# Kernel tuning notes

Hardware: AMD Instinct MI355X
Metric: run time of the kernel (lower is better)

## Reference

```python
import jax, jax.numpy as jnp
import numpy as np

N, E, F, H, L, G, EMB, C = 50000, 600000, 128, 128, 4, 64, 64, 10
BN_EPS = 1e-5


def setup_inputs() -> dict:
    key = jax.random.key(0)
    k = lambda i: jax.random.fold_in(key, i)
    s = 0.05  # weight scale
    return {
        "x": jax.random.normal(k(0), (N, F), jnp.float32),
        "edge_index": jax.random.randint(k(1), (2, E), 0, N, jnp.int64),
        "batch": jnp.sort(jax.random.randint(k(2), (N,), 0, G, jnp.int64)),
        "emb": jax.random.normal(k(3), (G, EMB), jnp.float32),
        "eps": jnp.zeros((L,), jnp.float32),
        "W1": jax.random.normal(k(4), (L, F, H), jnp.float32) * s,
        "b1": jnp.zeros((L, H), jnp.float32),
        "W2": jax.random.normal(k(5), (L, H, H), jnp.float32) * s,
        "b2": jnp.zeros((L, H), jnp.float32),
        "gamma": jnp.ones((L, H), jnp.float32),
        "beta": jnp.zeros((L, H), jnp.float32),
        "lin1_w": jax.random.normal(k(6), (L * H + EMB, 2 * H), jnp.float32) * s,
        "lin1_b": jnp.zeros((2 * H,), jnp.float32),
        "lin2_w": jax.random.normal(k(7), (2 * H, H), jnp.float32) * s,
        "lin2_b": jnp.zeros((H,), jnp.float32),
        "lin4_w": jax.random.normal(k(8), (H, C), jnp.float32) * s,
        "lin4_b": jnp.zeros((C,), jnp.float32),
    }


def _gin_mlp(h, W1, b1, W2, b2, gamma, beta):
    # Linear -> ReLU -> Linear -> ReLU -> BatchNorm1d (batch stats)
    h = jax.nn.relu(h @ W1 + b1)
    h = jax.nn.relu(h @ W2 + b2)
    mean = jnp.mean(h, axis=0)
    var = jnp.var(h, axis=0)
    return (h - mean) * jax.lax.rsqrt(var + BN_EPS) * gamma + beta


def reference(x, edge_index, batch, emb, eps, W1, b1, W2, b2, gamma, beta,
              lin1_w, lin1_b, lin2_w, lin2_b, lin4_w, lin4_b):
    src, dst = edge_index[0], edge_index[1]
    xs = []
    for l in range(L):
        # GIN: MLP((1+eps)*x_i + sum_{j->i} x_j)  via gather + scatter-add
        agg = jax.ops.segment_sum(x[src], dst, num_segments=N)  # [N,H]
        x = _gin_mlp((1.0 + eps[l]) * x + agg,
                     W1[l], b1[l], W2[l], b2[l], gamma[l], beta[l])
        xs.append(x)
    h = jnp.concatenate(xs, axis=1)  # [N, L*H]
    # global mean pool per graph
    sums = jax.ops.segment_sum(h, batch, num_segments=G)  # [G, L*H]
    cnt = jax.ops.segment_sum(jnp.ones((N,), h.dtype), batch, num_segments=G)
    pooled = sums / jnp.maximum(cnt, 1.0)[:, None]
    z = jnp.concatenate([pooled, emb.reshape(G, -1)], axis=1)
    z = jax.nn.relu(z @ lin1_w + lin1_b)  # .relu() twice is idempotent
    # dropout p=0.5 skipped (eval mode); lin3 unused in original forward
    z = jax.nn.relu(z @ lin2_w + lin2_b)
    z = z @ lin4_w + lin4_b
    return jax.nn.log_softmax(z, axis=1)
```

## Files before the change

### kernel.cpp

```cpp
#include <hip/hip_runtime.h>
#include <cstdint>
#include <cstddef>

#define N_NODES 50000
#define N_EDGES 600000
#define NLAYER  4
#define NGRAPH  64
#define STRIDE  64
#define NBANK   64
#define NBLK_MLP ((N_NODES + 127) / 128)
#define CVTX_NB ((N_NODES * 32 + 255) / 256)
#define CVTW_NB ((NLAYER * 128 * 128 * 2) / 256)
#define EDG_NB  ((N_EDGES + 255) / 256)

typedef unsigned int   u32;
typedef unsigned short u16;
typedef unsigned char  u8;
typedef float f32x4  __attribute__((ext_vector_type(4)));
typedef short bf16x8 __attribute__((ext_vector_type(8)));

__device__ __forceinline__ u16 f2bf(float f) {
    u32 x = __float_as_uint(f);
    u32 r = x + 0x7fffu + ((x >> 16) & 1u);
    return (u16)(r >> 16);
}
__device__ __forceinline__ u32 pack2(float a, float b) {
    return (u32)f2bf(a) | ((u32)f2bf(b) << 16);
}

__device__ __forceinline__ float fp8b0(u32 u) { return __builtin_amdgcn_cvt_f32_fp8(u, 0); }
__device__ __forceinline__ float fp8b1(u32 u) { return __builtin_amdgcn_cvt_f32_fp8(u, 1); }
__device__ __forceinline__ u32 pk_fp8(float a, float b) {
    return (u32)__builtin_amdgcn_cvt_pk_fp8_f32(a, b, 0, false);
}

__global__ __launch_bounds__(256) void setup_all(
    const float4* __restrict__ x, u32* __restrict__ xf8,
    const float* __restrict__ W1, const float* __restrict__ W2,
    short* __restrict__ W1t, short* __restrict__ W2t,
    const int* __restrict__ src, const int* __restrict__ dst,
    int* __restrict__ cnt, u16* __restrict__ col) {
    int b = blockIdx.x, tid = threadIdx.x;
    if (b < EDG_NB) {
        int e = b * 256 + tid;
        if (e < N_EDGES) {
            int d = dst[e];
            int pos = atomicAdd(&cnt[d], 1);
            if (pos < STRIDE) col[d * STRIDE + pos] = (u16)src[e];
        }
    } else if (b < EDG_NB + CVTX_NB) {
        int i = (b - EDG_NB) * 256 + tid;
        if (i < N_NODES * 32) {
            float4 v = x[i];
            u32 r = pk_fp8(v.x, v.y);
            r = (u32)__builtin_amdgcn_cvt_pk_fp8_f32(v.z, v.w, (int)r, true);
            xf8[i] = r;
        }
    } else {
        int i = (b - EDG_NB - CVTX_NB) * 256 + tid;
        int z = i >> 16, r = i & 65535;
        int l = r >> 14, n = (r >> 7) & 127, k = r & 127;
        const float* W = z ? W2 : W1;
        short* Wt      = z ? W2t : W1t;
        Wt[((size_t)l * 128 + n) * 128 + k] = (short)f2bf(W[((size_t)l * 128 + k) * 128 + n]);
    }
}

__global__ __launch_bounds__(256) void agg_kernel(
    const u16* __restrict__ xin,
    const float* __restrict__ coef,
    const int* __restrict__ cnt, const u16* __restrict__ col,
    const float* __restrict__ eps_all, int layer,
    u32* __restrict__ agg) {
    int node = blockIdx.x * 4 + (threadIdx.x >> 6);
    int lane = threadIdx.x & 63;
    if (node >= N_NODES) return;
    float a0 = 1.f, a1 = 1.f, d0 = 0.f, d1 = 0.f;
    if (coef) {
        a0 = coef[2 * lane];       a1 = coef[2 * lane + 1];
        d0 = coef[128 + 2 * lane]; d1 = coef[128 + 2 * lane + 1];
    }
    float ep = 1.0f + eps_all[layer];
    u32 v = xin[(size_t)node * 64 + lane];
    int dgc = min(cnt[node], STRIDE);
    int k0 = node * STRIDE, k1 = k0 + dgc;
    float s0 = 0.f, s1 = 0.f;
    int k = k0;
    int cc[8];
    if (k < k1) {
#pragma unroll
        for (int t = 0; t < 8; t++) cc[t] = col[min(k + t, k1 - 1)];
    }
    while (k < k1) {
        int idx[8];
#pragma unroll
        for (int t = 0; t < 8; t++) idx[t] = cc[t];
        int kn = k + 8;
        if (kn < k1) {
#pragma unroll
            for (int t = 0; t < 8; t++) cc[t] = col[min(kn + t, k1 - 1)];
        }
#pragma unroll
        for (int t = 0; t < 8; t++) {
            u32 u = xin[(size_t)idx[t] * 64 + lane];
            float w = (k + t < k1) ? 1.f : 0.f;
            s0 += w * fp8b0(u); s1 += w * fp8b1(u);
        }
        k = kn;
    }
    float deg = (float)dgc;
    float r0 = ep * (a0 * fp8b0(v) + d0) + a0 * s0 + deg * d0;
    float r1 = ep * (a1 * fp8b1(v) + d1) + a1 * s1 + deg * d1;
    agg[(size_t)node * 64 + lane] = pack2(r0, r1);
}

#define H1_STRIDE 136
#define WSTR      132
__global__ __launch_bounds__(256) void mlp_fused(
    const short* __restrict__ A,
    const short* __restrict__ W1t, const float* __restrict__ b1,
    const short* __restrict__ W2t, const float* __restrict__ b2,
    u8* __restrict__ H2, const int* __restrict__ batch,
    float* __restrict__ sumsB, float* __restrict__ gsum, int M) {
    __shared__ alignas(16) short wbuf[128 * WSTR];
    __shared__ alignas(16) short h1s[128 * H1_STRIDE];
    __shared__ int sh_ga, sh_gb, sh_split;
    int tid  = threadIdx.x;
    int wave = tid >> 6, lane = tid & 63;
    int ln15 = lane & 15, quad = lane >> 4;
    int m0blk = blockIdx.x * 128;
    int m0 = m0blk + wave * 32;
    const bf16x8 zz = {0, 0, 0, 0, 0, 0, 0, 0};

    if (tid == 0) {
        int rlo = m0blk, rhi = min(m0blk + 127, M - 1);
        int ga = batch[rlo], gb = batch[rhi];
        int split = m0blk + 128;
        if (ga != gb) {
            int lo = rlo, hi = rhi;
            while (lo + 1 < hi) { int mid = (lo + hi) >> 1; if (batch[mid] == ga) lo = mid; else hi = mid; }
            split = hi;
        }
        sh_ga = ga; sh_gb = gb; sh_split = split;
    }

    bf16x8 a[2][4];
#pragma unroll
    for (int rt = 0; rt < 2; rt++) {
        int row = m0 + rt * 16 + ln15;
        const short* rp = A + (size_t)row * 128 + quad * 8;
        bool ok = row < M;
#pragma unroll
        for (int s = 0; s < 4; s++)
            a[rt][s] = ok ? *(const bf16x8*)(rp + s * 32) : zz;
    }
    bf16x8 wr1[8], wr2[8];
#pragma unroll
    for (int i = 0; i < 8; i++)
        wr1[i] = *(const bf16x8*)(W1t + (size_t)(i * 256 + tid) * 8);
#pragma unroll
    for (int i = 0; i < 8; i++)
        wr2[i] = *(const bf16x8*)(W2t + (size_t)(i * 256 + tid) * 8);

#pragma unroll
    for (int i = 0; i < 8; i++) {
        int idx = i * 256 + tid;
        *(bf16x8*)&wbuf[(idx >> 4) * WSTR + (idx & 15) * 8] = wr1[i];
    }
    __syncthreads();

#pragma unroll
    for (int ct = 0; ct < 8; ct++) {
        const short* wp = &wbuf[(ct * 16 + ln15) * WSTR + quad * 8];
        bf16x8 b[4];
#pragma unroll
        for (int s = 0; s < 4; s++) b[s] = *(const bf16x8*)(wp + s * 32);
        float bias = b1[ct * 16 + ln15];
#pragma unroll
        for (int rt = 0; rt < 2; rt++) {
            f32x4 acc = {0.f, 0.f, 0.f, 0.f};
#pragma unroll
            for (int s = 0; s < 4; s++)
                acc = __builtin_amdgcn_mfma_f32_16x16x32_bf16(a[rt][s], b[s], acc, 0, 0, 0);
#pragma unroll
            for (int i = 0; i < 4; i++) {
                float v = fmaxf(acc[i] + bias, 0.f);
                int lr = wave * 32 + rt * 16 + quad * 4 + i;
                h1s[lr * H1_STRIDE + ct * 16 + ln15] = (short)f2bf(v);
            }
        }
    }
    __syncthreads();

#pragma unroll
    for (int i = 0; i < 8; i++) {
        int idx = i * 256 + tid;
        *(bf16x8*)&wbuf[(idx >> 4) * WSTR + (idx & 15) * 8] = wr2[i];
    }
    bf16x8 c[2][4];
#pragma unroll
    for (int rt = 0; rt < 2; rt++) {
        const short* rp = h1s + (size_t)(wave * 32 + rt * 16 + ln15) * H1_STRIDE + quad * 8;
#pragma unroll
        for (int s = 0; s < 4; s++) c[rt][s] = *(const bf16x8*)(rp + s * 32);
    }
    __syncthreads();

    int gsplit = sh_split;
    float sAcc[8], qAcc[8], pAcc[8];
#pragma unroll
    for (int ct = 0; ct < 8; ct++) { sAcc[ct] = 0.f; qAcc[ct] = 0.f; pAcc[ct] = 0.f; }
#pragma unroll
    for (int ct = 0; ct < 8; ct++) {
        const short* wp = &wbuf[(ct * 16 + ln15) * WSTR + quad * 8];
        bf16x8 b[4];
#pragma unroll
        for (int s = 0; s < 4; s++) b[s] = *(const bf16x8*)(wp + s * 32);
        float bias = b2[ct * 16 + ln15];
#pragma unroll
        for (int rt = 0; rt < 2; rt++) {
            f32x4 acc = {0.f, 0.f, 0.f, 0.f};
#pragma unroll
            for (int s = 0; s < 4; s++)
                acc = __builtin_amdgcn_mfma_f32_16x16x32_bf16(c[rt][s], b[s], acc, 0, 0, 0);
            int colx = ct * 16 + ln15;
#pragma unroll
            for (int i = 0; i < 4; i++) {
                int row = m0 + rt * 16 + quad * 4 + i;
                float v = fmaxf(acc[i] + bias, 0.f);
                if (row < M) H2[(size_t)row * 128 + colx] = (u8)(pk_fp8(v, v) & 0xffu);
                float vm = (row < M) ? v : 0.f;
                sAcc[ct] += vm; qAcc[ct] += vm * vm;
                if (row < gsplit) pAcc[ct] += vm;
            }
        }
    }
    __syncthreads();
    float* scr = (float*)h1s;
    int slice = wave * 4 + quad;
#pragma unroll
    for (int ct = 0; ct < 8; ct++) {
        int colx = ct * 16 + ln15;
        scr[(0 * 16 + slice) * 128 + colx] = sAcc[ct];
        scr[(1 * 16 + slice) * 128 + colx] = qAcc[ct];
        scr[(2 * 16 + slice) * 128 + colx] = pAcc[ct];
    }
    __syncthreads();
    if (tid < 128) {
        float ss = 0.f, qq = 0.f, pa = 0.f;
#pragma unroll
        for (int sl = 0; sl < 16; sl++) {
            ss += scr[(0 * 16 + sl) * 128 + tid];
            qq += scr[(1 * 16 + sl) * 128 + tid];
            pa += scr[(2 * 16 + sl) * 128 + tid];
        }
        float* sb = sumsB + (size_t)(blockIdx.x & (NBANK - 1)) * 256;
        atomicAdd(&sb[tid], ss);
        atomicAdd(&sb[128 + tid], qq);
        int ga = sh_ga, gb = sh_gb;
        atomicAdd(&gsum[ga * 128 + tid], pa);
        if (gb != ga) atomicAdd(&gsum[gb * 128 + tid], ss - pa);
    }
}

__global__ __launch_bounds__(128) void coef_fin(
    const float* __restrict__ sumsB,
    const float* __restrict__ gamma, const float* __restrict__ beta,
    int layer, float* __restrict__ coef) {
    int t = threadIdx.x;
    float s1 = 0.f, s2 = 0.f;
    for (int b = 0; b < NBANK; b++) {
        s1 += sumsB[b * 256 + t];
        s2 += sumsB[b * 256 + 128 + t];
    }
    float mean = s1 * (1.0f / N_NODES);
    float var  = s2 * (1.0f / N_NODES) - mean * mean;
    float a = rsqrtf(var + 1e-5f) * gamma[layer * 128 + t];
    coef[t]       = a;
    coef[128 + t] = beta[layer * 128 + t] - mean * a;
}

__global__ __launch_bounds__(256) void head_kernel(
    const float* __restrict__ gsum, const float* __restrict__ coefL,
    const int* __restrict__ batch, const float* __restrict__ emb,
    const float* __restrict__ l1w, const float* __restrict__ l1b,
    const float* __restrict__ l2w, const float* __restrict__ l2b,
    const float* __restrict__ l4w, const float* __restrict__ l4b,
    float* __restrict__ out) {
    __shared__ float z[576];
    __shared__ float z1[256];
    __shared__ float z2h[2][128];
    __shared__ float z2[128];
    __shared__ float zr[128][10];
    __shared__ float inv_cnt;
    int g = blockIdx.x;
    int tid = threadIdx.x;
    if (tid == 0) {
        int lo = 0, hi = N_NODES;
        while (lo < hi) { int m = (lo + hi) >> 1; if (batch[m] < g) lo = m + 1; else hi = m; }
        int s = lo;
        lo = 0; hi = N_NODES;
        while (lo < hi) { int m = (lo + hi) >> 1; if (batch[m] < g + 1) lo = m + 1; else hi = m; }
        inv_cnt = 1.0f / fmaxf((float)(lo - s), 1.0f);
    }
    __syncthreads();
    for (int j = tid; j < 512; j += 256) {
        int l = j >> 7, c = j & 127;
        float a = coefL[l * 256 + c], d = coefL[l * 256 + 128 + c];
        z[j] = a * gsum[(size_t)l * NGRAPH * 128 + g * 128 + c] * inv_cnt + d;
    }
    if (tid < 64) z[512 + tid] = emb[g * 64 + tid];
    __syncthreads();
    {
        float acc = l1b[tid];
        for (int j0 = 0; j0 < 576; j0 += 16) {
            float lw[16];
#pragma unroll
            for (int t = 0; t < 16; t++) lw[t] = l1w[(j0 + t) * 256 + tid];
#pragma unroll
            for (int t = 0; t < 16; t++) acc += z[j0 + t] * lw[t];
        }
        z1[tid] = fmaxf(acc, 0.f);
    }
    __syncthreads();
    {
        int c2 = tid & 127, half = tid >> 7;
        float acc = 0.f;
        int jb = half * 128;
        for (int j0 = 0; j0 < 128; j0 += 8) {
            float lw[8];
#pragma unroll
            for (int t = 0; t < 8; t++) lw[t] = l2w[(jb + j0 + t) * 128 + c2];
#pragma unroll
            for (int t = 0; t < 8; t++) acc += z1[jb + j0 + t] * lw[t];
        }
        z2h[half][c2] = acc;
    }
    __syncthreads();
    if (tid < 128) z2[tid] = fmaxf(z2h[0][tid] + z2h[1][tid] + l2b[tid], 0.f);
    __syncthreads();
    if (tid < 128) {
        float zv = z2[tid];
        const float* wr = l4w + tid * 10;
#pragma unroll
        for (int c = 0; c < 10; c++) zr[tid][c] = zv * wr[c];
    }
    __syncthreads();
    for (int s = 64; s >= 1; s >>= 1) {
        if (tid < s) {
#pragma unroll
            for (int c = 0; c < 10; c++) zr[tid][c] += zr[tid + s][c];
        }
        __syncthreads();
    }
    if (tid == 0) {
        float z3s[10];
#pragma unroll
        for (int c = 0; c < 10; c++) z3s[c] = zr[0][c] + l4b[c];
        float m = z3s[0];
        for (int i = 1; i < 10; i++) m = fmaxf(m, z3s[i]);
        float se = 0.f;
        for (int i = 0; i < 10; i++) se += expf(z3s[i] - m);
        float lse = m + logf(se);
        for (int i = 0; i < 10; i++) out[g * 10 + i] = z3s[i] - lse;
    }
}

extern "C" void kernel_launch(void* const* d_in, const int* in_sizes, int n_in,
                              void* d_out, int out_size, void* d_ws, size_t ws_size,
                              hipStream_t stream) {
    (void)in_sizes; (void)n_in; (void)out_size; (void)ws_size;
    const float* x0   = (const float*)d_in[0];
    const int* ei     = (const int*)d_in[1];
    const int* src    = ei;
    const int* dst    = ei + N_EDGES;
    const int* batch  = (const int*)d_in[2];
    const float* emb  = (const float*)d_in[3];
    const float* eps  = (const float*)d_in[4];
    const float* W1   = (const float*)d_in[5];
    const float* b1   = (const float*)d_in[6];
    const float* W2   = (const float*)d_in[7];
    const float* b2   = (const float*)d_in[8];
    const float* gamma= (const float*)d_in[9];
    const float* beta = (const float*)d_in[10];
    const float* l1w  = (const float*)d_in[11];
    const float* l1b  = (const float*)d_in[12];
    const float* l2w  = (const float*)d_in[13];
    const float* l2b  = (const float*)d_in[14];
    const float* l4w  = (const float*)d_in[15];
    const float* l4b  = (const float*)d_in[16];

    char* ws = (char*)d_ws;
    size_t off = 0;
    auto alloc = [&](size_t bytes) -> char* {
        char* p = ws + off; off += (bytes + 255) & ~(size_t)255; return p;
    };
    int* cnt    = (int*)alloc(N_NODES * 4);
    float* sumsB = (float*)alloc((size_t)NLAYER * NBANK * 256 * 4);
    float* gsumL = (float*)alloc((size_t)NLAYER * NGRAPH * 128 * 4);
    size_t zero_len = (char*)gsumL - (char*)cnt + (size_t)NLAYER * NGRAPH * 128 * 4;
    u16* col    = (u16*)alloc((size_t)N_NODES * STRIDE * 2);
    u8* xf8     = (u8*)alloc((size_t)N_NODES * 128);
    u8* h2a     = (u8*)alloc((size_t)N_NODES * 128);
    u8* h2b     = (u8*)alloc((size_t)N_NODES * 128);
    u32* agg    = (u32*)alloc((size_t)N_NODES * 64 * 4);
    short* W1t  = (short*)alloc((size_t)NLAYER * 128 * 128 * 2);
    short* W2t  = (short*)alloc((size_t)NLAYER * 128 * 128 * 2);
    float* coefL = (float*)alloc(NLAYER * 256 * 4);

    hipMemsetAsync(cnt, 0, zero_len, stream);

    setup_all<<<EDG_NB + CVTX_NB + CVTW_NB, 256, 0, stream>>>(
        (const float4*)x0, (u32*)xf8, W1, W2, W1t, W2t, src, dst, cnt, col);

    const u8* xin = xf8;
    for (int l = 0; l < NLAYER; ++l) {
        u8* h2 = (l & 1) ? h2b : h2a;
        const float* coef_prev = (l == 0) ? nullptr : (coefL + (l - 1) * 256);
        agg_kernel<<<(N_NODES + 3) / 4, 256, 0, stream>>>(
            (const u16*)xin, coef_prev, cnt, col, eps, l, agg);
        mlp_fused<<<NBLK_MLP, 256, 0, stream>>>(
            (const short*)agg, W1t + (size_t)l * 16384, b1 + l * 128,
            W2t + (size_t)l * 16384, b2 + l * 128, h2, batch,
            sumsB + (size_t)l * NBANK * 256, gsumL + (size_t)l * NGRAPH * 128, N_NODES);
        coef_fin<<<1, 128, 0, stream>>>(sumsB + (size_t)l * NBANK * 256,
                                        gamma, beta, l, coefL + l * 256);
        xin = h2;
    }
    head_kernel<<<NGRAPH, 256, 0, stream>>>(gsumL, coefL, batch, emb,
                                            l1w, l1b, l2w, l2b, l4w, l4b,
                                            (float*)d_out);
}
```

Measured before the change: 378.5 us.

## Split wave into four neighbor groups with 8-byte gathers and shuffle reduction

The aggregation kernel now has each wave work on four neighbor rows at once. Each 16-lane group gathers one 128-byte fp8 row using 8-byte loads, and the groups sum their partial results with xor shuffles. Before, the whole wave read a single row with 2-byte loads per lane, so the new layout issues fewer, wider gather instructions and keeps more memory requests in flight. The costs are extra shuffle work, more registers per lane, and only a quarter of the lanes doing the final wider store.

```diff
diff --git a/kernel.cpp b/kernel.cpp
--- a/kernel.cpp
+++ b/kernel.cpp
@@ -18,6 +18,8 @@
 typedef unsigned char  u8;
 typedef float f32x4  __attribute__((ext_vector_type(4)));
 typedef short bf16x8 __attribute__((ext_vector_type(8)));
+typedef u32 u32x2 __attribute__((ext_vector_type(2)));
+typedef u32 u32x4 __attribute__((ext_vector_type(4)));
 
 __device__ __forceinline__ u16 f2bf(float f) {
     u32 x = __float_as_uint(f);
@@ -32,6 +34,14 @@
 __device__ __forceinline__ float fp8b1(u32 u) { return __builtin_amdgcn_cvt_f32_fp8(u, 1); }
 __device__ __forceinline__ u32 pk_fp8(float a, float b) {
     return (u32)__builtin_amdgcn_cvt_pk_fp8_f32(a, b, 0, false);
+}
+__device__ __forceinline__ float fp8b(u32 u, int j) {
+    switch (j) {
+    case 0:  return __builtin_amdgcn_cvt_f32_fp8(u, 0);
+    case 1:  return __builtin_amdgcn_cvt_f32_fp8(u, 1);
+    case 2:  return __builtin_amdgcn_cvt_f32_fp8(u, 2);
+    default: return __builtin_amdgcn_cvt_f32_fp8(u, 3);
+    }
 }
 
 __global__ __launch_bounds__(256) void setup_all(
@@ -67,7 +77,7 @@
 }
 
 __global__ __launch_bounds__(256) void agg_kernel(
-    const u16* __restrict__ xin,
+    const u8* __restrict__ xin,
     const float* __restrict__ coef,
     const int* __restrict__ cnt, const u16* __restrict__ col,
     const float* __restrict__ eps_all, int layer,
@@ -75,43 +85,88 @@
     int node = blockIdx.x * 4 + (threadIdx.x >> 6);
     int lane = threadIdx.x & 63;
     if (node >= N_NODES) return;
-    float a0 = 1.f, a1 = 1.f, d0 = 0.f, d1 = 0.f;
+    int g  = lane >> 4;
+    int ch = lane & 15;
+
+    float A[8], D[8];
     if (coef) {
-        a0 = coef[2 * lane];       a1 = coef[2 * lane + 1];
-        d0 = coef[128 + 2 * lane]; d1 = coef[128 + 2 * lane + 1];
+#pragma unroll
+        for (int j = 0; j < 8; j++) {
+            A[j] = coef[ch * 8 + j];
+            D[j] = coef[128 + ch * 8 + j];
+        }
+    } else {
+#pragma unroll
+        for (int j = 0; j < 8; j++) { A[j] = 1.f; D[j] = 0.f; }
     }
     float ep = 1.0f + eps_all[layer];
-    u32 v = xin[(size_t)node * 64 + lane];
+    const u8* rowbase = xin + ch * 8;
     int dgc = min(cnt[node], STRIDE);
     int k0 = node * STRIDE, k1 = k0 + dgc;
-    float s0 = 0.f, s1 = 0.f;
+    float s[8];
+#pragma unroll
+    for (int j = 0; j < 8; j++) s[j] = 0.f;
+
+    int cc[4]; u32x2 rr[4];
     int k = k0;
-    int cc[8];
     if (k < k1) {
 #pragma unroll
-        for (int t = 0; t < 8; t++) cc[t] = col[min(k + t, k1 - 1)];
+        for (int t = 0; t < 4; t++) cc[t] = col[min(k + t * 4 + g, k1 - 1)];
+#pragma unroll
+        for (int t = 0; t < 4; t++) rr[t] = *(const u32x2*)(rowbase + (size_t)cc[t] * 128);
     }
     while (k < k1) {
-        int idx[8];
-#pragma unroll
-        for (int t = 0; t < 8; t++) idx[t] = cc[t];
-        int kn = k + 8;
-        if (kn < k1) {
-#pragma unroll
-            for (int t = 0; t < 8; t++) cc[t] = col[min(kn + t, k1 - 1)];
-        }
-#pragma unroll
-        for (int t = 0; t < 8; t++) {
-            u32 u = xin[(size_t)idx[t] * 64 + lane];
-            float w = (k + t < k1) ? 1.f : 0.f;
-            s0 += w * fp8b0(u); s1 += w * fp8b1(u);
+        int kn = k + 16;
+        bool more = kn < k1;
+        int c2[4];
+        if (more) {
+#pragma unroll
+            for (int t = 0; t < 4; t++) c2[t] = col[min(kn + t * 4 + g, k1 - 1)];
+        }
+        u32 u[8];
+#pragma unroll
+        for (int t = 0; t < 4; t++) {
+            bool ok = (k + t * 4 + g) < k1;
+            u[2 * t]     = ok ? rr[t].x : 0u;
+            u[2 * t + 1] = ok ? rr[t].y : 0u;
+        }
+        if (more) {
+#pragma unroll
+            for (int t = 0; t < 4; t++) rr[t] = *(const u32x2*)(rowbase + (size_t)c2[t] * 128);
+        }
+#pragma unroll
+        for (int t = 0; t < 4; t++) {
+#pragma unroll
+            for (int j = 0; j < 4; j++) {
+                s[j]     += fp8b(u[2 * t],     j);
+                s[4 + j] += fp8b(u[2 * t + 1], j);
+            }
         }
         k = kn;
     }
+#pragma unroll
+    for (int j = 0; j < 8; j++) {
+        s[j] += __shfl_xor(s[j], 16);
+        s[j] += __shfl_xor(s[j], 32);
+    }
+    u32x2 sv = *(const u32x2*)(rowbase + (size_t)node * 128);
     float deg = (float)dgc;
-    float r0 = ep * (a0 * fp8b0(v) + d0) + a0 * s0 + deg * d0;
-    float r1 = ep * (a1 * fp8b1(v) + d1) + a1 * s1 + deg * d1;
-    agg[(size_t)node * 64 + lane] = pack2(r0, r1);
+    float r[8];
+#pragma unroll
+    for (int j = 0; j < 4; j++) {
+        float x0 = fp8b(sv.x, j);
+        float x1 = fp8b(sv.y, j);
+        r[j]     = ep * (A[j]     * x0 + D[j])     + A[j]     * s[j]     + deg * D[j];
+        r[4 + j] = ep * (A[4 + j] * x1 + D[4 + j]) + A[4 + j] * s[4 + j] + deg * D[4 + j];
+    }
+    if (g == 0) {
+        u32x4 o;
+        o.x = pack2(r[0], r[1]);
+        o.y = pack2(r[2], r[3]);
+        o.z = pack2(r[4], r[5]);
+        o.w = pack2(r[6], r[7]);
+        *(u32x4*)(agg + (size_t)node * 64 + ch * 4) = o;
+    }
 }
 
 #define H1_STRIDE 136
@@ -418,7 +473,7 @@
         u8* h2 = (l & 1) ? h2b : h2a;
         const float* coef_prev = (l == 0) ? nullptr : (coefL + (l - 1) * 256);
         agg_kernel<<<(N_NODES + 3) / 4, 256, 0, stream>>>(
-            (const u16*)xin, coef_prev, cnt, col, eps, l, agg);
+            xin, coef_prev, cnt, col, eps, l, agg);
         mlp_fused<<<NBLK_MLP, 256, 0, stream>>>(
             (const short*)agg, W1t + (size_t)l * 16384, b1 + l * 128,
             W2t + (size_t)l * 16384, b2 + l * 128, h2, batch,
```

Measured after the change: 403.3 us. 6.5% more time.
